# Performance work log

Hardware: AMD Instinct MI355X
Metric: run time of the kernel (lower is better)

The kernel has to match this reference:

```python
import jax, jax.numpy as jnp
import numpy as np

GROUPS = 32  # from analyze_enhance_linear_ops(4096, 4096, 0.05): smallest divisor g with 1/g <= 0.05


def setup_inputs() -> dict:
    key = jax.random.key(0)
    k1, k2, k3, k4, k5 = jax.random.split(key, 5)
    B, S, D_in, D_out = 4, 2048, 4096, 4096
    ig = D_out // GROUPS  # 128
    x = jax.random.normal(k1, (B, S, D_in), dtype=jnp.float32)
    W = jax.random.normal(k2, (D_out, D_in), dtype=jnp.float32) * 0.02
    b = jax.random.normal(k3, (D_out,), dtype=jnp.float32) * 0.02
    Wg = jax.random.normal(k4, (GROUPS, ig, ig), dtype=jnp.float32) * 0.02
    bg = jax.random.normal(k5, (GROUPS, ig), dtype=jnp.float32) * 0.02
    return {"x": x, "W": W, "b": b, "Wg": Wg, "bg": bg}


def reference(x, W, b, Wg, bg):
    # original_linear: dense GEMM, torch Linear layout W[out, in]
    y = jnp.einsum('bsi,oi->bso', x, W) + b            # [B, S, D_out]
    # GroupedLinear: block-diagonal transform over groups of size out_group
    B, S, D = y.shape
    G, og, ig = Wg.shape
    yg = y.reshape(B, S, G, ig)                        # split into groups
    out = jnp.einsum('bsgi,goi->bsgo', yg, Wg) + bg    # per-group small GEMM + bias
    return out.reshape(B, S, D)                        # cat along feature dim
```

## Files before the change

kernel.cpp:

```cpp
#include <hip/hip_runtime.h>
#include <hip/hip_bf16.h>
#include <stdint.h>

typedef float f32x4 __attribute__((ext_vector_type(4)));
typedef short s16x8 __attribute__((ext_vector_type(8)));
typedef unsigned int u32x2 __attribute__((ext_vector_type(2)));
typedef unsigned int u32x4 __attribute__((ext_vector_type(4)));

#define MDIM 8192
#define NDIM 4096
#define KDIM 4096
#define NKT  64

__device__ __forceinline__ unsigned pkbf(float lo, float hi) {
  unsigned short l = __builtin_bit_cast(unsigned short, __float2bfloat16(lo));
  unsigned short h = __builtin_bit_cast(unsigned short, __float2bfloat16(hi));
  return ((unsigned)h << 16) | (unsigned)l;
}

__device__ __forceinline__ void gload16(const void* g, void* l) {
  __builtin_amdgcn_global_load_lds((const __attribute__((address_space(1))) int*)g,
                                   (__attribute__((address_space(3))) int*)l, 16, 0, 0);
}

__global__ __launch_bounds__(256) void conv_tile(
    const float* __restrict__ X, const float* __restrict__ W,
    s16x8* __restrict__ wsA, s16x8* __restrict__ wsB) {
  __shared__ char lds[32768];
  const int b = blockIdx.x;
  const int tid = threadIdx.x;
  const float* src;
  s16x8* dst;
  int bi;
  if (b < 32 * NKT) { src = X; dst = wsA; bi = b; }
  else              { src = W; dst = wsB; bi = b - 32 * NKT; }
  const int rt = bi >> 6;
  const int kt = bi & 63;
  const int fr = tid >> 4;
  const int c4 = (tid & 15) * 4;
  const int h = c4 >> 5, q = (c4 >> 3) & 3, eh = (c4 >> 2) & 1;
  #pragma unroll
  for (int f = 0; f < 16; ++f) {
    const int row = f * 16 + fr;
    f32x4 v = *(const f32x4*)(src + ((size_t)rt * 256 + row) * KDIM + kt * 64 + c4);
    u32x2 p = { pkbf(v[0], v[1]), pkbf(v[2], v[3]) };
    *(u32x2*)(lds + (h * 16 + f) * 1024 + (q * 16 + fr) * 16 + eh * 8) = p;
  }
  __syncthreads();
  const size_t ob = (size_t)bi * 2048;
  #pragma unroll
  for (int i = 0; i < 8; ++i)
    dst[ob + i * 256 + tid] = *(const s16x8*)(lds + (i * 256 + tid) * 16);
}

__global__ __launch_bounds__(512, 2) void gemm256(
    const s16x8* __restrict__ wsA, const s16x8* __restrict__ wsB,
    const float* __restrict__ bias, const float* __restrict__ Wg,
    const float* __restrict__ bg, float* __restrict__ out) {
  extern __shared__ char smem[];
  const int tid = threadIdx.x;
  const int lane = tid & 63;
  const int wid = tid >> 6;
  const int wr = wid >> 2;
  const int wc = wid & 3;
  const int fr = lane & 15;
  const int q4 = lane >> 4;

  const int bid = blockIdx.x;
  const int swz = (bid & 7) * 64 + (bid >> 3);
  const int bm = swz >> 4;
  const int bn = swz & 15;

  const size_t aBase = (size_t)bm * NKT * 2048;
  const size_t bBase = (size_t)bn * NKT * 2048;

  auto stage = [&](int kt, int db, int isB, int h) {
    const s16x8* s = (isB ? wsB + bBase : wsA + aBase)
                     + (size_t)kt * 2048 + h * 1024 + wid * 128 + lane;
    char* d = smem + isB * 65536 + db * 32768 + h * 16384 + wid * 2048;
    gload16(s, d);
    gload16(s + 64, d + 1024);
  };

  const char* aRd = smem + wr * 8192 + lane * 16;
  const char* bRd = smem + 65536 + wc * 4096 + lane * 16;

  f32x4 acc[8][4];
  #pragma unroll
  for (int m = 0; m < 8; ++m)
    #pragma unroll
    for (int n = 0; n < 4; ++n) acc[m][n] = (f32x4)0.0f;

  s16x8 af[8], bfr[4];

#define SP(DB, H, SKT, SDB, SH)                                                \
  {                                                                            \
    stage(SKT, SDB, 0, SH);                                                    \
    stage(SKT, SDB, 1, SH);                                                    \
    _Pragma("unroll")                                                          \
    for (int n = 0; n < 4; ++n)                                                \
      bfr[n] = *(const s16x8*)(bRd + (DB)*32768 + (H)*16384 + n * 1024);       \
    _Pragma("unroll")                                                          \
    for (int m = 0; m < 8; ++m)                                                \
      af[m] = *(const s16x8*)(aRd + (DB)*32768 + (H)*16384 + m * 1024);        \
    asm volatile("s_waitcnt vmcnt(8)" ::: "memory");                           \
    __builtin_amdgcn_s_barrier();                                              \
    asm volatile("s_waitcnt lgkmcnt(4)" ::: "memory");                         \
    __builtin_amdgcn_s_setprio(1);                                             \
    _Pragma("unroll")                                                          \
    for (int m = 0; m < 4; ++m) {                                              \
      _Pragma("unroll")                                                        \
      for (int n = 0; n < 4; ++n)                                              \
        acc[m][n] = __builtin_amdgcn_mfma_f32_16x16x32_bf16(                   \
            af[m], bfr[n], acc[m][n], 0, 0, 0);                                \
    }                                                                          \
    asm volatile("s_waitcnt lgkmcnt(0)" ::: "memory");                         \
    _Pragma("unroll")                                                          \
    for (int m = 4; m < 8; ++m) {                                              \
      _Pragma("unroll")                                                        \
      for (int n = 0; n < 4; ++n)                                              \
        acc[m][n] = __builtin_amdgcn_mfma_f32_16x16x32_bf16(                   \
            af[m], bfr[n], acc[m][n], 0, 0, 0);                                \
    }                                                                          \
    __builtin_amdgcn_s_setprio(0);                                             \
    __builtin_amdgcn_s_barrier();                                              \
  }

  stage(0, 0, 0, 0); stage(0, 0, 1, 0);
  stage(0, 0, 0, 1); stage(0, 0, 1, 1);
  stage(1, 1, 0, 0); stage(1, 1, 1, 0);
  asm volatile("s_waitcnt vmcnt(8)" ::: "memory");
  __builtin_amdgcn_s_barrier();

  #pragma clang loop unroll(disable)
  for (int it = 0; it < 32; ++it) {
    const int u0 = 2 * it;
    const int k1 = u0 + 1;
    const int k2 = (u0 + 2 < NKT) ? u0 + 2 : NKT - 1;
    const int k3 = (u0 + 3 < NKT) ? u0 + 3 : NKT - 1;
    SP(0, 0, k1, 1, 1)
    SP(0, 1, k2, 0, 0)
    SP(1, 0, k2, 0, 1)
    SP(1, 1, k3, 1, 0)
  }
#undef SP

  asm volatile("s_waitcnt vmcnt(0)" ::: "memory");
  asm volatile("s_waitcnt lgkmcnt(0)" ::: "memory");
  __builtin_amdgcn_s_barrier();

  float bv[4];
  #pragma unroll
  for (int n = 0; n < 4; ++n) bv[n] = bias[bn * 256 + wc * 64 + n * 16 + fr];

  #pragma unroll
  for (int m = 0; m < 8; ++m) {
    const int Mf = wr * 8 + m;
    #pragma unroll
    for (int np = 0; np < 2; ++np) {
      const int Kh = wc * 2 + np;
      #pragma unroll
      for (int j = 0; j < 8; ++j) {
        const int nn = np * 2 + (j >> 2);
        const int r = (j + q4) & 3;
        const int qq = (j >> 2) * 2 + (fr >> 3);
        const int frs = q4 * 4 + r;
        const float y = acc[m][nn][r] + bv[nn];
        *(unsigned short*)(smem + (Mf * 8 + Kh) * 1024 + (qq * 16 + frs) * 16 + (fr & 7) * 2)
            = __builtin_bit_cast(unsigned short, __float2bfloat16(y));
      }
    }
  }
  asm volatile("s_waitcnt lgkmcnt(0)" ::: "memory");
  __builtin_amdgcn_s_barrier();

  const int g = bn * 2 + (wc >> 1);
  const float* wgb = Wg + (size_t)g * 16384;
  f32x4 acc2[8][4];
  #pragma unroll
  for (int m = 0; m < 8; ++m)
    #pragma unroll
    for (int n = 0; n < 4; ++n) acc2[m][n] = (f32x4)0.0f;

  #pragma unroll
  for (int s = 0; s < 4; ++s) {
    const int Kh = (wc >> 1) * 4 + s;
    s16x8 af2[8];
    #pragma unroll
    for (int m = 0; m < 8; ++m)
      af2[m] = *(const s16x8*)(smem + ((wr * 8 + m) * 8 + Kh) * 1024 + lane * 16);
    #pragma unroll
    for (int n = 0; n < 4; ++n) {
      const int ocl = (wc & 1) * 64 + n * 16 + fr;
      const float* wp = wgb + ocl * 128 + s * 32 + q4 * 8;
      f32x4 w0 = *(const f32x4*)wp;
      f32x4 w1 = *(const f32x4*)(wp + 4);
      u32x4 pw = { pkbf(w0[0], w0[1]), pkbf(w0[2], w0[3]),
                   pkbf(w1[0], w1[1]), pkbf(w1[2], w1[3]) };
      const s16x8 bfw = __builtin_bit_cast(s16x8, pw);
      #pragma unroll
      for (int m = 0; m < 8; ++m)
        acc2[m][n] = __builtin_amdgcn_mfma_f32_16x16x32_bf16(af2[m], bfw, acc2[m][n], 0, 0, 0);
    }
  }

  float bgv[4];
  #pragma unroll
  for (int n = 0; n < 4; ++n) bgv[n] = bg[bn * 256 + wc * 64 + n * 16 + fr];

  #pragma unroll
  for (int m = 0; m < 8; ++m) {
    #pragma unroll
    for (int n = 0; n < 4; ++n) {
      const int col = bn * 256 + wc * 64 + n * 16 + fr;
      #pragma unroll
      for (int r = 0; r < 4; ++r) {
        const size_t row = (size_t)bm * 256 + wr * 128 + m * 16 + q4 * 4 + r;
        out[row * NDIM + col] = acc2[m][n][r] + bgv[n];
      }
    }
  }
}

extern "C" void kernel_launch(void* const* d_in, const int* in_sizes, int n_in,
                              void* d_out, int out_size, void* d_ws, size_t ws_size,
                              hipStream_t stream) {
  const float* X    = (const float*)d_in[0];
  const float* W    = (const float*)d_in[1];
  const float* bias = (const float*)d_in[2];
  const float* Wg   = (const float*)d_in[3];
  const float* bg   = (const float*)d_in[4];
  float* out = (float*)d_out;

  s16x8* wsA = (s16x8*)d_ws;
  s16x8* wsB = wsA + ((size_t)MDIM * KDIM / 8);

  hipFuncSetAttribute(reinterpret_cast<const void*>(gemm256),
                      hipFuncAttributeMaxDynamicSharedMemorySize, 131072);

  conv_tile<<<dim3(3072), dim3(256), 0, stream>>>(X, W, wsA, wsB);
  gemm256<<<dim3(512), dim3(512), 131072, stream>>>(wsA, wsB, bias, Wg, bg, out);
}
```

Baseline: 301.8 us.

## Switch GEMMs to 32x32x16 MFMA with matching fragment layout and finer pipeline

New measurement: 310.3 us. +2.8%, slower.

```diff
diff --git a/kernel.cpp b/kernel.cpp
--- a/kernel.cpp
+++ b/kernel.cpp
@@ -3,6 +3,7 @@
 #include <stdint.h>
 
 typedef float f32x4 __attribute__((ext_vector_type(4)));
+typedef float f32x16 __attribute__((ext_vector_type(16)));
 typedef short s16x8 __attribute__((ext_vector_type(8)));
 typedef unsigned int u32x2 __attribute__((ext_vector_type(2)));
 typedef unsigned int u32x4 __attribute__((ext_vector_type(4)));
@@ -38,13 +39,18 @@
   const int kt = bi & 63;
   const int fr = tid >> 4;
   const int c4 = (tid & 15) * 4;
-  const int h = c4 >> 5, q = (c4 >> 3) & 3, eh = (c4 >> 2) & 1;
+  const int h = c4 >> 5;
+  const int ks2 = (c4 >> 4) & 1;
+  const int lh = (c4 & 15) >> 3;
+  const int e2 = (c4 & 7) * 2;
   #pragma unroll
   for (int f = 0; f < 16; ++f) {
     const int row = f * 16 + fr;
     f32x4 v = *(const f32x4*)(src + ((size_t)rt * 256 + row) * KDIM + kt * 64 + c4);
     u32x2 p = { pkbf(v[0], v[1]), pkbf(v[2], v[3]) };
-    *(u32x2*)(lds + (h * 16 + f) * 1024 + (q * 16 + fr) * 16 + eh * 8) = p;
+    const int frag = (h * 2 + ks2) * 8 + (f >> 1);
+    const int lane = lh * 32 + (f & 1) * 16 + fr;
+    *(u32x2*)(lds + frag * 1024 + lane * 16 + e2) = p;
   }
   __syncthreads();
   const size_t ob = (size_t)bi * 2048;
@@ -63,8 +69,8 @@
   const int wid = tid >> 6;
   const int wr = wid >> 2;
   const int wc = wid & 3;
-  const int fr = lane & 15;
-  const int q4 = lane >> 4;
+  const int c32 = lane & 31;
+  const int q5 = lane >> 5;
 
   const int bid = blockIdx.x;
   const int swz = (bid & 7) * 64 + (bid >> 3);
@@ -82,54 +88,44 @@
     gload16(s + 64, d + 1024);
   };
 
-  const char* aRd = smem + wr * 8192 + lane * 16;
-  const char* bRd = smem + 65536 + wc * 4096 + lane * 16;
-
-  f32x4 acc[8][4];
-  #pragma unroll
-  for (int m = 0; m < 8; ++m)
-    #pragma unroll
-    for (int n = 0; n < 4; ++n) acc[m][n] = (f32x4)0.0f;
-
-  s16x8 af[8], bfr[4];
-
-#define SP(DB, H, SKT, SDB, SH)                                                \
+  const char* aRd = smem + wr * 4096 + lane * 16;
+  const char* bRd = smem + 65536 + wc * 2048 + lane * 16;
+
+  f32x16 acc[4][2];
+  #pragma unroll
+  for (int m = 0; m < 4; ++m)
+    #pragma unroll
+    for (int n = 0; n < 2; ++n) acc[m][n] = (f32x16)0.0f;
+
+  s16x8 af[4], bfr[2];
+
+#define SP(DB, H, KS2, SKT, SDB, SOP, SH, DOVM)                                \
   {                                                                            \
-    stage(SKT, SDB, 0, SH);                                                    \
-    stage(SKT, SDB, 1, SH);                                                    \
+    stage(SKT, SDB, SOP, SH);                                                  \
     _Pragma("unroll")                                                          \
-    for (int n = 0; n < 4; ++n)                                                \
-      bfr[n] = *(const s16x8*)(bRd + (DB)*32768 + (H)*16384 + n * 1024);       \
+    for (int n = 0; n < 2; ++n)                                                \
+      bfr[n] = *(const s16x8*)(bRd + (DB)*32768 + (H)*16384 + (KS2)*8192 + n * 1024); \
     _Pragma("unroll")                                                          \
-    for (int m = 0; m < 8; ++m)                                                \
-      af[m] = *(const s16x8*)(aRd + (DB)*32768 + (H)*16384 + m * 1024);        \
-    asm volatile("s_waitcnt vmcnt(8)" ::: "memory");                           \
+    for (int m = 0; m < 4; ++m)                                                \
+      af[m] = *(const s16x8*)(aRd + (DB)*32768 + (H)*16384 + (KS2)*8192 + m * 1024);  \
+    if (DOVM) asm volatile("s_waitcnt vmcnt(4)" ::: "memory");                 \
     __builtin_amdgcn_s_barrier();                                              \
-    asm volatile("s_waitcnt lgkmcnt(4)" ::: "memory");                         \
+    asm volatile("s_waitcnt lgkmcnt(0)" ::: "memory");                         \
     __builtin_amdgcn_s_setprio(1);                                             \
     _Pragma("unroll")                                                          \
     for (int m = 0; m < 4; ++m) {                                              \
       _Pragma("unroll")                                                        \
-      for (int n = 0; n < 4; ++n)                                              \
-        acc[m][n] = __builtin_amdgcn_mfma_f32_16x16x32_bf16(                   \
-            af[m], bfr[n], acc[m][n], 0, 0, 0);                                \
-    }                                                                          \
-    asm volatile("s_waitcnt lgkmcnt(0)" ::: "memory");                         \
-    _Pragma("unroll")                                                          \
-    for (int m = 4; m < 8; ++m) {                                              \
-      _Pragma("unroll")                                                        \
-      for (int n = 0; n < 4; ++n)                                              \
-        acc[m][n] = __builtin_amdgcn_mfma_f32_16x16x32_bf16(                   \
+      for (int n = 0; n < 2; ++n)                                              \
+        acc[m][n] = __builtin_amdgcn_mfma_f32_32x32x16_bf16(                   \
             af[m], bfr[n], acc[m][n], 0, 0, 0);                                \
     }                                                                          \
     __builtin_amdgcn_s_setprio(0);                                             \
-    __builtin_amdgcn_s_barrier();                                              \
   }
 
   stage(0, 0, 0, 0); stage(0, 0, 1, 0);
   stage(0, 0, 0, 1); stage(0, 0, 1, 1);
   stage(1, 1, 0, 0); stage(1, 1, 1, 0);
-  asm volatile("s_waitcnt vmcnt(8)" ::: "memory");
+  asm volatile("s_waitcnt vmcnt(4)" ::: "memory");
   __builtin_amdgcn_s_barrier();
 
   #pragma clang loop unroll(disable)
@@ -138,10 +134,14 @@
     const int k1 = u0 + 1;
     const int k2 = (u0 + 2 < NKT) ? u0 + 2 : NKT - 1;
     const int k3 = (u0 + 3 < NKT) ? u0 + 3 : NKT - 1;
-    SP(0, 0, k1, 1, 1)
-    SP(0, 1, k2, 0, 0)
-    SP(1, 0, k2, 0, 1)
-    SP(1, 1, k3, 1, 0)
+    SP(0, 0, 0, k1, 1, 0, 1, 0)
+    SP(0, 0, 1, k1, 1, 1, 1, 0)
+    SP(0, 1, 0, k2, 0, 0, 0, 0)
+    SP(0, 1, 1, k2, 0, 1, 0, 1)
+    SP(1, 0, 0, k2, 0, 0, 1, 0)
+    SP(1, 0, 1, k2, 0, 1, 1, 0)
+    SP(1, 1, 0, k3, 1, 0, 0, 0)
+    SP(1, 1, 1, k3, 1, 1, 0, 1)
   }
 #undef SP
 
@@ -149,25 +149,27 @@
   asm volatile("s_waitcnt lgkmcnt(0)" ::: "memory");
   __builtin_amdgcn_s_barrier();
 
-  float bv[4];
-  #pragma unroll
-  for (int n = 0; n < 4; ++n) bv[n] = bias[bn * 256 + wc * 64 + n * 16 + fr];
-
-  #pragma unroll
-  for (int m = 0; m < 8; ++m) {
-    const int Mf = wr * 8 + m;
-    #pragma unroll
-    for (int np = 0; np < 2; ++np) {
-      const int Kh = wc * 2 + np;
+  float bv[2];
+  #pragma unroll
+  for (int n = 0; n < 2; ++n) bv[n] = bias[bn * 256 + wc * 64 + n * 32 + c32];
+
+  {
+    const int e2 = (c32 & 7) * 2;
+    const int lh = (c32 >> 3) & 1;
+    #pragma unroll
+    for (int m = 0; m < 4; ++m) {
+      const int Mf = wr * 4 + m;
       #pragma unroll
-      for (int j = 0; j < 8; ++j) {
-        const int nn = np * 2 + (j >> 2);
-        const int r = (j + q4) & 3;
-        const int qq = (j >> 2) * 2 + (fr >> 3);
-        const int frs = q4 * 4 + r;
-        const float y = acc[m][nn][r] + bv[nn];
-        *(unsigned short*)(smem + (Mf * 8 + Kh) * 1024 + (qq * 16 + frs) * 16 + (fr & 7) * 2)
-            = __builtin_bit_cast(unsigned short, __float2bfloat16(y));
+      for (int n = 0; n < 2; ++n) {
+        const int Kc = wc * 4 + n * 2 + (c32 >> 4);
+        char* base = smem + (Mf * 16 + Kc) * 1024 + lh * 512 + e2;
+        #pragma unroll
+        for (int r = 0; r < 16; ++r) {
+          const int rl = (r & 3) + 8 * (r >> 2) + 4 * q5;
+          const float y = acc[m][n][r] + bv[n];
+          *(unsigned short*)(base + rl * 16) =
+              __builtin_bit_cast(unsigned short, __float2bfloat16(y));
+        }
       }
     }
   }
@@ -176,46 +178,47 @@
 
   const int g = bn * 2 + (wc >> 1);
   const float* wgb = Wg + (size_t)g * 16384;
-  f32x4 acc2[8][4];
-  #pragma unroll
-  for (int m = 0; m < 8; ++m)
-    #pragma unroll
-    for (int n = 0; n < 4; ++n) acc2[m][n] = (f32x4)0.0f;
-
-  #pragma unroll
-  for (int s = 0; s < 4; ++s) {
-    const int Kh = (wc >> 1) * 4 + s;
-    s16x8 af2[8];
-    #pragma unroll
-    for (int m = 0; m < 8; ++m)
-      af2[m] = *(const s16x8*)(smem + ((wr * 8 + m) * 8 + Kh) * 1024 + lane * 16);
-    #pragma unroll
-    for (int n = 0; n < 4; ++n) {
-      const int ocl = (wc & 1) * 64 + n * 16 + fr;
-      const float* wp = wgb + ocl * 128 + s * 32 + q4 * 8;
+  f32x16 acc2[4][2];
+  #pragma unroll
+  for (int m = 0; m < 4; ++m)
+    #pragma unroll
+    for (int n = 0; n < 2; ++n) acc2[m][n] = (f32x16)0.0f;
+
+  #pragma unroll
+  for (int ks = 0; ks < 8; ++ks) {
+    const int Kc = (wc >> 1) * 8 + ks;
+    s16x8 af2[4];
+    #pragma unroll
+    for (int m = 0; m < 4; ++m)
+      af2[m] = *(const s16x8*)(smem + ((wr * 4 + m) * 16 + Kc) * 1024 + lane * 16);
+    #pragma unroll
+    for (int n = 0; n < 2; ++n) {
+      const int ocl = (wc & 1) * 64 + n * 32 + c32;
+      const float* wp = wgb + ocl * 128 + ks * 16 + q5 * 8;
       f32x4 w0 = *(const f32x4*)wp;
       f32x4 w1 = *(const f32x4*)(wp + 4);
       u32x4 pw = { pkbf(w0[0], w0[1]), pkbf(w0[2], w0[3]),
                    pkbf(w1[0], w1[1]), pkbf(w1[2], w1[3]) };
       const s16x8 bfw = __builtin_bit_cast(s16x8, pw);
       #pragma unroll
-      for (int m = 0; m < 8; ++m)
-        acc2[m][n] = __builtin_amdgcn_mfma_f32_16x16x32_bf16(af2[m], bfw, acc2[m][n], 0, 0, 0);
+      for (int m = 0; m < 4; ++m)
+        acc2[m][n] = __builtin_amdgcn_mfma_f32_32x32x16_bf16(af2[m], bfw, acc2[m][n], 0, 0, 0);
     }
   }
 
-  float bgv[4];
-  #pragma unroll
-  for (int n = 0; n < 4; ++n) bgv[n] = bg[bn * 256 + wc * 64 + n * 16 + fr];
-
-  #pragma unroll
-  for (int m = 0; m < 8; ++m) {
-    #pragma unroll
-    for (int n = 0; n < 4; ++n) {
-      const int col = bn * 256 + wc * 64 + n * 16 + fr;
+  float bgv[2];
+  #pragma unroll
+  for (int n = 0; n < 2; ++n) bgv[n] = bg[bn * 256 + wc * 64 + n * 32 + c32];
+
+  #pragma unroll
+  for (int m = 0; m < 4; ++m) {
+    #pragma unroll
+    for (int n = 0; n < 2; ++n) {
+      const int col = bn * 256 + wc * 64 + n * 32 + c32;
       #pragma unroll
-      for (int r = 0; r < 4; ++r) {
-        const size_t row = (size_t)bm * 256 + wr * 128 + m * 16 + q4 * 4 + r;
+      for (int r = 0; r < 16; ++r) {
+        const size_t row = (size_t)bm * 256 + wr * 128 + m * 32
+                         + (r & 3) + 8 * (r >> 2) + 4 * q5;
         out[row * NDIM + col] = acc2[m][n][r] + bgv[n];
       }
     }
```
